# Optimization experiments

Measured on AMD Instinct MI355X. Metric: run time of the kernel, lower is better.

Reference implementation:

```python
import jax, jax.numpy as jnp
import numpy as np

MARGIN = 0.8
EPS = 1e-6  # torch F.pairwise_distance eps added to the difference


def setup_inputs() -> dict:
    key = jax.random.key(0)
    k1, k2, k3 = jax.random.split(key, 3)
    B, D = 8192, 128
    emb = jax.random.normal(k1, (B, D), dtype=jnp.float32)
    labels = jax.random.randint(k2, (B,), 0, 6)
    sbj = jax.random.randint(k3, (B,), 0, 16)
    return {"emb": emb, "labels": labels, "sbj": sbj}


def reference(emb, labels, sbj):
    B = emb.shape[0]
    # Squared pairwise distances (monotone in true distance -> same argmax/argmin)
    sq = jnp.sum(emb * emb, axis=1)
    d2 = sq[:, None] + sq[None, :] - 2.0 * (emb @ emb.T)  # [B, B]
    same_s = sbj[:, None] == sbj[None, :]
    same_l = labels[:, None] == labels[None, :]
    eye = jnp.eye(B, dtype=bool)
    pos_m = same_s & same_l & ~eye          # within-subject, same label, not self
    neg_m = same_s & ~same_l                # within-subject, different label
    valid = pos_m.any(axis=1) & neg_m.any(axis=1)
    p_idx = jnp.argmax(jnp.where(pos_m, d2, -jnp.inf), axis=1)  # hardest positive
    n_idx = jnp.argmin(jnp.where(neg_m, d2, jnp.inf), axis=1)   # hardest negative
    # TripletMarginLoss(p=2): pairwise_distance adds eps to the difference
    dap = jnp.linalg.norm(emb - emb[p_idx] + EPS, axis=1)
    dan = jnp.linalg.norm(emb - emb[n_idx] + EPS, axis=1)
    per = jnp.maximum(dap - dan + MARGIN, 0.0)
    cnt = jnp.sum(valid)
    loss = jnp.sum(jnp.where(valid, per, 0.0)) / jnp.maximum(cnt, 1)
    return jnp.where(cnt > 0, loss, 0.0)
```

## Files before the change

### kernel.cpp

```cpp
#include <hip/hip_runtime.h>
#include <math.h>
#include <limits.h>

#define D 128
#define NSUBJ 16
#define MAXN 640
#define MARGIN 0.8f
#define PRB 32
#define TI 16
#define TJ 64
#define NSTRIPE 32
#define NBLK (NSUBJ * NSTRIPE)

typedef __attribute__((ext_vector_type(8))) short bf16x8;
typedef __attribute__((ext_vector_type(4))) float f32x4;

static __device__ __forceinline__ short f2bf(float f) {
    union { float f; unsigned u; } v; v.f = f;
    unsigned r = v.u + 0x7FFF + ((v.u >> 16) & 1);
    return (short)(r >> 16);
}

__global__ __launch_bounds__(256) void prep_kernel(
        const float* __restrict__ emb, const int* __restrict__ labels,
        const int* __restrict__ sbj, int* __restrict__ counts,
        int4* __restrict__ pmeta, short* __restrict__ ebf, int B) {
    __shared__ int s_cnt[NSUBJ], s_base[NSUBJ], s_slot[PRB];
    const int t = threadIdx.x, bid = blockIdx.x;
    if (t < NSUBJ) s_cnt[t] = 0;
    __syncthreads();
    int s = 0, mypos = 0;
    if (t < PRB) { s = sbj[bid * PRB + t]; mypos = atomicAdd(&s_cnt[s], 1); }
    __syncthreads();
    if (t < NSUBJ) s_base[t] = atomicAdd(&counts[t], s_cnt[t]);
    __syncthreads();
    if (t < PRB) {
        int pos = s_base[s] + mypos;
        s_slot[t] = (pos < MAXN) ? (s * MAXN + pos) : -1;
    }
    __syncthreads();
#pragma unroll
    for (int it = 0; it < (PRB * 16) / 256; ++it) {
        int lin = it * 256 + t;
        int row = lin >> 4, u = lin & 15;
        int i = bid * PRB + row;
        int slot = s_slot[row];
        const float4* rp = (const float4*)(emb + (size_t)i * D);
        float4 a0 = rp[u * 2], a1 = rp[u * 2 + 1];
        float ssq = 0.f;
        ssq = fmaf(a0.x, a0.x, ssq); ssq = fmaf(a0.y, a0.y, ssq);
        ssq = fmaf(a0.z, a0.z, ssq); ssq = fmaf(a0.w, a0.w, ssq);
        ssq = fmaf(a1.x, a1.x, ssq); ssq = fmaf(a1.y, a1.y, ssq);
        ssq = fmaf(a1.z, a1.z, ssq); ssq = fmaf(a1.w, a1.w, ssq);
#pragma unroll
        for (int off = 8; off > 0; off >>= 1) ssq += __shfl_down(ssq, off, 16);
        if (slot >= 0) {
            bf16x8 pk;
            pk[0] = f2bf(a0.x); pk[1] = f2bf(a0.y); pk[2] = f2bf(a0.z); pk[3] = f2bf(a0.w);
            pk[4] = f2bf(a1.x); pk[5] = f2bf(a1.y); pk[6] = f2bf(a1.z); pk[7] = f2bf(a1.w);
            *(bf16x8*)&ebf[(size_t)slot * D + u * 8] = pk;
            if (u == 0)
                pmeta[slot] = make_int4(labels[i], i, __float_as_int(ssq), 0);
        }
    }
}

#define LOADTILE(B0, B1, B2, B3, MI, ML, MS, JT)                         \
    do {                                                                 \
        int jl_ = (JT) * TJ + w * 16 + c, cl_ = min(jl_, n - 1);         \
        const short* rp_ = ebf + (size_t)(base + cl_) * D;               \
        B0 = *(const bf16x8*)&rp_[q * 8];                                \
        B1 = *(const bf16x8*)&rp_[32 + q * 8];                           \
        B2 = *(const bf16x8*)&rp_[64 + q * 8];                           \
        B3 = *(const bf16x8*)&rp_[96 + q * 8];                           \
        int4 m_ = pmeta[base + cl_];                                     \
        MI = (jl_ < n) ? m_.y : -1; ML = m_.x; MS = __int_as_float(m_.z);\
    } while (0)

#define STEP(B0, B1, B2, B3, MI, ML, MS)                                 \
    do {                                                                 \
        f32x4 acc = {0.f, 0.f, 0.f, 0.f};                                \
        acc = __builtin_amdgcn_mfma_f32_16x16x32_bf16(afr[0], B0, acc, 0, 0, 0); \
        acc = __builtin_amdgcn_mfma_f32_16x16x32_bf16(afr[1], B1, acc, 0, 0, 0); \
        acc = __builtin_amdgcn_mfma_f32_16x16x32_bf16(afr[2], B2, acc, 0, 0, 0); \
        acc = __builtin_amdgcn_mfma_f32_16x16x32_bf16(afr[3], B3, acc, 0, 0, 0); \
        if ((MI) >= 0) {                                                 \
            _Pragma("unroll")                                            \
            for (int r = 0; r < 4; ++r) {                                \
                float v = fmaf(-2.f, acc[r], (MS));                      \
                if ((ML) == li[r]) {                                     \
                    if ((MI) != gI[r] && v > vP[r]) { vP[r] = v; iP[r] = (MI); } \
                } else if (v < vN[r]) { vN[r] = v; iN[r] = (MI); }       \
            }                                                            \
        }                                                                \
    } while (0)

__global__ __launch_bounds__(256) void triplet_kernel(
        const short* __restrict__ ebf, const int4* __restrict__ pmeta,
        const int* __restrict__ counts,
        float* __restrict__ loss_sum, int* __restrict__ valid_cnt,
        int* __restrict__ done, float* __restrict__ out) {
    const int bid = blockIdx.x, t = threadIdx.x;
    const int s = bid & 15;
    const int stripe = bid >> 4;
    const int base = s * MAXN;
    const int n = min(counts[s], MAXN);
    const int lane = t & 63, w = t >> 6, c = lane & 15, q = lane >> 4;

    __shared__ float svP[TI][4]; __shared__ int siP[TI][4];
    __shared__ float svN[TI][4]; __shared__ int siN[TI][4];

    float blockSum = 0.f; int blockCnt = 0;

    for (int i0 = stripe * TI; i0 < n; i0 += NSTRIPE * TI) {
        const int nrows = min(TI, n - i0);

        bf16x8 afr[4];
        {
            const short* ap = ebf + (size_t)(base + i0 + min(c, nrows - 1)) * D;
#pragma unroll
            for (int st = 0; st < 4; ++st)
                afr[st] = *(const bf16x8*)&ap[st * 32 + q * 8];
        }
        int li[4], gI[4];
#pragma unroll
        for (int r = 0; r < 4; ++r) {
            int row = q * 4 + r;
            if (row < nrows) { int4 m = pmeta[base + i0 + row]; li[r] = m.x; gI[r] = m.y; }
            else             { li[r] = INT_MIN; gI[r] = -1; }
        }

        float vP[4], vN[4]; int iP[4], iN[4];
#pragma unroll
        for (int r = 0; r < 4; ++r) {
            vP[r] = -INFINITY; iP[r] = -1;
            vN[r] =  INFINITY; iN[r] = -1;
        }

        const int ntiles = (n + TJ - 1) / TJ;
        bf16x8 b00, b01, b02, b03, b10, b11, b12, b13;
        int mi0 = -1, ml0 = INT_MIN, mi1 = -1, ml1 = INT_MIN;
        float ms0 = 0.f, ms1 = 0.f;
        if (0 < ntiles) LOADTILE(b00, b01, b02, b03, mi0, ml0, ms0, 0);
        if (1 < ntiles) LOADTILE(b10, b11, b12, b13, mi1, ml1, ms1, 1);

        for (int jt = 0; jt < ntiles; jt += 2) {
            {
                bf16x8 c0 = b00, c1 = b01, c2 = b02, c3 = b03;
                int cmi = mi0, cml = ml0; float cms = ms0;
                if (jt + 2 < ntiles) LOADTILE(b00, b01, b02, b03, mi0, ml0, ms0, jt + 2);
                STEP(c0, c1, c2, c3, cmi, cml, cms);
            }
            if (jt + 1 < ntiles) {
                bf16x8 c0 = b10, c1 = b11, c2 = b12, c3 = b13;
                int cmi = mi1, cml = ml1; float cms = ms1;
                if (jt + 3 < ntiles) LOADTILE(b10, b11, b12, b13, mi1, ml1, ms1, jt + 3);
                STEP(c0, c1, c2, c3, cmi, cml, cms);
            }
        }

#pragma unroll
        for (int off = 8; off > 0; off >>= 1) {
#pragma unroll
            for (int r = 0; r < 4; ++r) {
                float ov = __shfl_down(vP[r], off, 16);
                int   oi = __shfl_down(iP[r], off, 16);
                if (ov > vP[r] || (ov == vP[r] && (unsigned)oi < (unsigned)iP[r])) {
                    vP[r] = ov; iP[r] = oi;
                }
                float on = __shfl_down(vN[r], off, 16);
                int   oj = __shfl_down(iN[r], off, 16);
                if (on < vN[r] || (on == vN[r] && (unsigned)oj < (unsigned)iN[r])) {
                    vN[r] = on; iN[r] = oj;
                }
            }
        }
        if (c == 0) {
#pragma unroll
            for (int r = 0; r < 4; ++r) {
                int row = q * 4 + r;
                svP[row][w] = vP[r]; siP[row][w] = iP[r];
                svN[row][w] = vN[r]; siN[row][w] = iN[r];
            }
        }
        __syncthreads();

        if (t < TI) {
            float bp = svP[t][0]; int ip = siP[t][0];
            float bn = svN[t][0]; int in_ = siN[t][0];
#pragma unroll
            for (int ww = 1; ww < 4; ++ww) {
                float o = svP[t][ww]; int oi = siP[t][ww];
                if (o > bp || (o == bp && (unsigned)oi < (unsigned)ip)) { bp = o; ip = oi; }
                float on = svN[t][ww]; int oj = siN[t][ww];
                if (on < bn || (on == bn && (unsigned)oj < (unsigned)in_)) { bn = on; in_ = oj; }
            }
            bool valid = (t < nrows) && (ip >= 0) && (in_ >= 0);
            float sqi = __int_as_float(pmeta[base + i0 + min(t, nrows - 1)].z);
            float per = 0.f;
            if (valid) {
                float dap = sqrtf(fmaxf(bp + sqi, 0.f));
                float dan = sqrtf(fmaxf(bn + sqi, 0.f));
                per = fmaxf(dap - dan + MARGIN, 0.f);
            }
            int vc = valid ? 1 : 0;
#pragma unroll
            for (int off = 8; off > 0; off >>= 1) {
                per += __shfl_down(per, off, 16);
                vc  += __shfl_down(vc,  off, 16);
            }
            if (t == 0) { blockSum += per; blockCnt += vc; }
        }
        if (i0 + NSTRIPE * TI < n) __syncthreads();
    }

    if (t == 0) {
        if (blockCnt > 0) {
            atomicAdd(loss_sum, blockSum);
            atomicAdd(valid_cnt, blockCnt);
        }
        __threadfence();
        int ticket = atomicAdd(done, 1);
        if (ticket == NBLK - 1) {
            float sum = atomicAdd(loss_sum, 0.0f);
            int   cnt = atomicAdd(valid_cnt, 0);
            out[0] = (cnt > 0) ? (sum / (float)cnt) : 0.0f;
        }
    }
}

extern "C" void kernel_launch(void* const* d_in, const int* in_sizes, int n_in,
                              void* d_out, int out_size, void* d_ws, size_t ws_size,
                              hipStream_t stream) {
    const float* emb    = (const float*)d_in[0];
    const int*   labels = (const int*)d_in[1];
    const int*   sbj    = (const int*)d_in[2];
    float*       out    = (float*)d_out;
    int B = in_sizes[1];

    char*  ws        = (char*)d_ws;
    int*   counts    = (int*)ws;
    float* loss_sum  = (float*)(ws + 64);
    int*   valid_cnt = (int*)(ws + 72);
    int*   done      = (int*)(ws + 80);
    int4*  pmeta     = (int4*)(ws + 128);
    size_t ebf_off   = (128 + (size_t)NSUBJ * MAXN * sizeof(int4) + 255) & ~(size_t)255;
    short* ebf       = (short*)(ws + ebf_off);

    hipMemsetAsync(ws, 0, 128, stream);
    prep_kernel<<<B / PRB, 256, 0, stream>>>(emb, labels, sbj, counts, pmeta, ebf, B);
    triplet_kernel<<<NBLK, 256, 0, stream>>>(ebf, pmeta, counts,
                                             loss_sum, valid_cnt, done, out);
}
```

Baseline: 105.7 us.

## Use deterministic histogram+scan bucketing and deepen triplet tile prefetch to four

Replaces per-block global atomic slot allocation in prep with a separate histogram kernel and a single-block scan, so bucket positions are deterministic and contention-free. The triplet kernel's register prefetch pipeline goes from two to four tiles in flight, and it gets a launch-bounds occupancy hint of two blocks per CU. The cost is two extra kernel launches and higher register pressure from the extra prefetch buffers.

New measurement: 110.0 us. 1.04x slower.

```diff
diff --git a/kernel.cpp b/kernel.cpp
--- a/kernel.cpp
+++ b/kernel.cpp
@@ -7,6 +7,7 @@
 #define MAXN 640
 #define MARGIN 0.8f
 #define PRB 32
+#define NPB 256
 #define TI 16
 #define TJ 64
 #define NSTRIPE 32
@@ -21,21 +22,51 @@
     return (short)(r >> 16);
 }
 
+__global__ __launch_bounds__(64) void hist_kernel(const int* __restrict__ sbj,
+                                                  int* __restrict__ hist) {
+    __shared__ int s_cnt[NSUBJ];
+    const int t = threadIdx.x, bid = blockIdx.x;
+    if (t < NSUBJ) s_cnt[t] = 0;
+    __syncthreads();
+    if (t < PRB) atomicAdd(&s_cnt[sbj[bid * PRB + t]], 1);
+    __syncthreads();
+    if (t < NSUBJ) hist[bid * NSUBJ + t] = s_cnt[t];
+}
+
+__global__ __launch_bounds__(1024) void scan_kernel(const int* __restrict__ hist,
+                                                    int* __restrict__ hbase,
+                                                    int* __restrict__ counts) {
+    const int w = threadIdx.x >> 6;
+    const int l = threadIdx.x & 63;
+    int carry = 0;
+#pragma unroll
+    for (int k = 0; k < NPB / 64; ++k) {
+        int v = hist[(k * 64 + l) * NSUBJ + w];
+        int x = v;
+#pragma unroll
+        for (int off = 1; off < 64; off <<= 1) {
+            int o = __shfl_up(x, off, 64);
+            if (l >= off) x += o;
+        }
+        hbase[(k * 64 + l) * NSUBJ + w] = carry + (x - v);
+        carry += __shfl(x, 63, 64);
+    }
+    if (l == 0) counts[w] = carry;
+}
+
 __global__ __launch_bounds__(256) void prep_kernel(
         const float* __restrict__ emb, const int* __restrict__ labels,
-        const int* __restrict__ sbj, int* __restrict__ counts,
+        const int* __restrict__ sbj, const int* __restrict__ hbase,
         int4* __restrict__ pmeta, short* __restrict__ ebf, int B) {
-    __shared__ int s_cnt[NSUBJ], s_base[NSUBJ], s_slot[PRB];
+    __shared__ int s_cnt[NSUBJ], s_slot[PRB];
     const int t = threadIdx.x, bid = blockIdx.x;
     if (t < NSUBJ) s_cnt[t] = 0;
     __syncthreads();
     int s = 0, mypos = 0;
     if (t < PRB) { s = sbj[bid * PRB + t]; mypos = atomicAdd(&s_cnt[s], 1); }
     __syncthreads();
-    if (t < NSUBJ) s_base[t] = atomicAdd(&counts[t], s_cnt[t]);
-    __syncthreads();
     if (t < PRB) {
-        int pos = s_base[s] + mypos;
+        int pos = hbase[bid * NSUBJ + s] + mypos;
         s_slot[t] = (pos < MAXN) ? (s * MAXN + pos) : -1;
     }
     __syncthreads();
@@ -95,7 +126,7 @@
         }                                                                \
     } while (0)
 
-__global__ __launch_bounds__(256) void triplet_kernel(
+__global__ __launch_bounds__(256, 2) void triplet_kernel(
         const short* __restrict__ ebf, const int4* __restrict__ pmeta,
         const int* __restrict__ counts,
         float* __restrict__ loss_sum, int* __restrict__ valid_cnt,
@@ -139,22 +170,38 @@
 
         const int ntiles = (n + TJ - 1) / TJ;
         bf16x8 b00, b01, b02, b03, b10, b11, b12, b13;
+        bf16x8 b20, b21, b22, b23, b30, b31, b32, b33;
         int mi0 = -1, ml0 = INT_MIN, mi1 = -1, ml1 = INT_MIN;
-        float ms0 = 0.f, ms1 = 0.f;
+        int mi2 = -1, ml2 = INT_MIN, mi3 = -1, ml3 = INT_MIN;
+        float ms0 = 0.f, ms1 = 0.f, ms2 = 0.f, ms3 = 0.f;
         if (0 < ntiles) LOADTILE(b00, b01, b02, b03, mi0, ml0, ms0, 0);
         if (1 < ntiles) LOADTILE(b10, b11, b12, b13, mi1, ml1, ms1, 1);
-
-        for (int jt = 0; jt < ntiles; jt += 2) {
+        if (2 < ntiles) LOADTILE(b20, b21, b22, b23, mi2, ml2, ms2, 2);
+        if (3 < ntiles) LOADTILE(b30, b31, b32, b33, mi3, ml3, ms3, 3);
+
+        for (int jt = 0; jt < ntiles; jt += 4) {
             {
                 bf16x8 c0 = b00, c1 = b01, c2 = b02, c3 = b03;
                 int cmi = mi0, cml = ml0; float cms = ms0;
-                if (jt + 2 < ntiles) LOADTILE(b00, b01, b02, b03, mi0, ml0, ms0, jt + 2);
+                if (jt + 4 < ntiles) LOADTILE(b00, b01, b02, b03, mi0, ml0, ms0, jt + 4);
                 STEP(c0, c1, c2, c3, cmi, cml, cms);
             }
             if (jt + 1 < ntiles) {
                 bf16x8 c0 = b10, c1 = b11, c2 = b12, c3 = b13;
                 int cmi = mi1, cml = ml1; float cms = ms1;
-                if (jt + 3 < ntiles) LOADTILE(b10, b11, b12, b13, mi1, ml1, ms1, jt + 3);
+                if (jt + 5 < ntiles) LOADTILE(b10, b11, b12, b13, mi1, ml1, ms1, jt + 5);
+                STEP(c0, c1, c2, c3, cmi, cml, cms);
+            }
+            if (jt + 2 < ntiles) {
+                bf16x8 c0 = b20, c1 = b21, c2 = b22, c3 = b23;
+                int cmi = mi2, cml = ml2; float cms = ms2;
+                if (jt + 6 < ntiles) LOADTILE(b20, b21, b22, b23, mi2, ml2, ms2, jt + 6);
+                STEP(c0, c1, c2, c3, cmi, cml, cms);
+            }
+            if (jt + 3 < ntiles) {
+                bf16x8 c0 = b30, c1 = b31, c2 = b32, c3 = b33;
+                int cmi = mi3, cml = ml3; float cms = ms3;
+                if (jt + 7 < ntiles) LOADTILE(b30, b31, b32, b33, mi3, ml3, ms3, jt + 7);
                 STEP(c0, c1, c2, c3, cmi, cml, cms);
             }
         }
@@ -243,12 +290,17 @@
     float* loss_sum  = (float*)(ws + 64);
     int*   valid_cnt = (int*)(ws + 72);
     int*   done      = (int*)(ws + 80);
-    int4*  pmeta     = (int4*)(ws + 128);
-    size_t ebf_off   = (128 + (size_t)NSUBJ * MAXN * sizeof(int4) + 255) & ~(size_t)255;
+    int*   hist      = (int*)(ws + 128);
+    int*   hbase     = (int*)(ws + 128 + NPB * NSUBJ * sizeof(int));
+    size_t pmeta_off = (128 + 2 * (size_t)NPB * NSUBJ * sizeof(int) + 255) & ~(size_t)255;
+    int4*  pmeta     = (int4*)(ws + pmeta_off);
+    size_t ebf_off   = (pmeta_off + (size_t)NSUBJ * MAXN * sizeof(int4) + 255) & ~(size_t)255;
     short* ebf       = (short*)(ws + ebf_off);
 
     hipMemsetAsync(ws, 0, 128, stream);
-    prep_kernel<<<B / PRB, 256, 0, stream>>>(emb, labels, sbj, counts, pmeta, ebf, B);
+    hist_kernel<<<B / PRB, 64, 0, stream>>>(sbj, hist);
+    scan_kernel<<<1, 1024, 0, stream>>>(hist, hbase, counts);
+    prep_kernel<<<B / PRB, 256, 0, stream>>>(emb, labels, sbj, hbase, pmeta, ebf, B);
     triplet_kernel<<<NBLK, 256, 0, stream>>>(ebf, pmeta, counts,
                                              loss_sum, valid_cnt, done, out);
 }
```
